# Kernel tuning notes

Hardware: AMD Instinct MI355X
Metric: run time of the kernel (lower is better)

Reference implementation:

```python
import jax, jax.numpy as jnp
import numpy as np

HEADS = 8
DIM_HEAD = 32
SCALE = DIM_HEAD ** -0.5


def setup_inputs() -> dict:
    key = jax.random.key(0)
    k1, k2, k3 = jax.random.split(key, 3)
    B, H, W, C = 16, 64, 64, 256
    hidden = HEADS * DIM_HEAD  # 256
    x = jax.random.normal(k1, (B, H, W, C), dtype=jnp.float32)
    # 1x1 convs with no bias == dense matmuls over channel dim (glorot-ish scale)
    w_qkv = jax.random.normal(k2, (C, 3 * hidden), dtype=jnp.float32) * (1.0 / np.sqrt(C))
    w_out = jax.random.normal(k3, (hidden, C), dtype=jnp.float32) * (1.0 / np.sqrt(hidden))
    return {"x": x, "w_qkv": w_qkv, "w_out": w_out}


def reference(x, w_qkv, w_out):
    B, H, W, C = x.shape
    n = H * W
    # to_qkv: 1x1 conv, no bias
    qkv = jnp.einsum('bhwc,cf->bhwf', x, w_qkv)  # [B,H,W,3*hidden]
    q, k, v = jnp.split(qkv, 3, axis=-1)

    def to_heads(t):
        # 'b x y (h c) -> b h c (x y)'
        t = t.reshape(B, n, HEADS, DIM_HEAD)
        return jnp.transpose(t, (0, 2, 3, 1))  # [B, heads, dim_head, n]

    q, k, v = to_heads(q), to_heads(k), to_heads(v)
    q = jax.nn.softmax(q, axis=-2) * SCALE      # softmax over feature dim d
    k = jax.nn.softmax(k, axis=-1)              # softmax over spatial dim n
    context = jnp.einsum('bhdn,bhen->bhde', k, v)   # [B, heads, d, e]
    out = jnp.einsum('bhde,bhdn->bhen', context, q)  # [B, heads, e, n]
    # 'b h c (x y) -> b x y (h c)'
    out = jnp.transpose(out, (0, 3, 1, 2)).reshape(B, H, W, HEADS * DIM_HEAD)
    # to_out: 1x1 conv, no bias
    return jnp.einsum('bhwf,fc->bhwc', out, w_out)
```

## Files before the change

kernel.cpp:

```cpp
#include <hip/hip_runtime.h>

using short8 = __attribute__((ext_vector_type(8))) short;
using f32x4  = __attribute__((ext_vector_type(4))) float;

#define SCALE_Q 0.17677669529663687f
#define NCHUNK 16

__device__ __forceinline__ unsigned short f2bf(float f) {
  unsigned u = __float_as_uint(f);
  return (unsigned short)((u + 0x7FFFu + ((u >> 16) & 1u)) >> 16);
}
__device__ __forceinline__ float bf2f(unsigned h) { return __uint_as_float(h << 16); }

__device__ __forceinline__ void bf8_to_f(uint4 r, float* o) {
  o[0] = bf2f(r.x & 0xffffu); o[1] = bf2f(r.x >> 16);
  o[2] = bf2f(r.y & 0xffffu); o[3] = bf2f(r.y >> 16);
  o[4] = bf2f(r.z & 0xffffu); o[5] = bf2f(r.z >> 16);
  o[6] = bf2f(r.w & 0xffffu); o[7] = bf2f(r.w >> 16);
}

__global__ __launch_bounds__(256) void prep_kernel(
    const float* __restrict__ x, const float* __restrict__ wqkv, const float* __restrict__ wout,
    unsigned short* __restrict__ xb, unsigned short* __restrict__ wqkvT,
    unsigned short* __restrict__ woutT) {
  const int blk = blockIdx.x;
  if (blk < 16384) {
    const size_t i = ((size_t)blk * 256 + threadIdx.x) * 4;
    const float4 v = *(const float4*)(x + i);
    *(ushort4*)(xb + i) = make_ushort4(f2bf(v.x), f2bf(v.y), f2bf(v.z), f2bf(v.w));
  } else if (blk < 16384 + 768) {
    const int n = blk - 16384, k = threadIdx.x;
    wqkvT[n * 256 + k] = f2bf(wqkv[(size_t)k * 768 + n]);
  } else {
    const int c = blk - 16384 - 768, f = threadIdx.x;
    woutT[c * 256 + f] = f2bf(wout[(size_t)f * 256 + c]);
  }
}

__global__ __launch_bounds__(256) void gemm_qkv(
    const unsigned short* __restrict__ A, const unsigned short* __restrict__ BT,
    unsigned short* __restrict__ KV, unsigned short* __restrict__ QS, int K) {
  __shared__ unsigned short As[2][128][40];
  __shared__ unsigned short Bs[2][128][40];
  const int cpx = (int)gridDim.x >> 3;
  const int lin = ((int)blockIdx.x & 7) * cpx + ((int)blockIdx.x >> 3);
  const int bn = lin % 6, bm = lin / 6;
  const int tid = threadIdx.x, lane = tid & 63, wid = tid >> 6;
  const int wr = wid >> 1, wc = wid & 1;
  const int fr = lane & 15, hi = lane >> 4, fk = hi * 8;
  f32x4 acc[4][4] = {};
  const size_t abase = (size_t)bm * 128 * K;
  const size_t bbase = (size_t)bn * 128 * K;

  const int srow = tid >> 2, skc = (tid & 3) * 8;
  uint4 ra0, ra1, rb0, rb1;
  const unsigned short* Ap = A + abase + (size_t)srow * K + skc;
  const unsigned short* Bp = BT + bbase + (size_t)srow * K + skc;

  ra0 = *(const uint4*)(Ap);            ra1 = *(const uint4*)(Ap + (size_t)64 * K);
  rb0 = *(const uint4*)(Bp);            rb1 = *(const uint4*)(Bp + (size_t)64 * K);
  *(uint4*)&As[0][srow][skc] = ra0;     *(uint4*)&As[0][srow + 64][skc] = ra1;
  *(uint4*)&Bs[0][srow][skc] = rb0;     *(uint4*)&Bs[0][srow + 64][skc] = rb1;
  __syncthreads();

  const int ktiles = K >> 5;
  int cur = 0;
  for (int t = 0; t < ktiles; ++t) {
    if (t + 1 < ktiles) {
      const int kt = (t + 1) * 32;
      ra0 = *(const uint4*)(Ap + kt);     ra1 = *(const uint4*)(Ap + (size_t)64 * K + kt);
      rb0 = *(const uint4*)(Bp + kt);     rb1 = *(const uint4*)(Bp + (size_t)64 * K + kt);
    }
    short8 af[4], bfv[4];
#pragma unroll
    for (int i = 0; i < 4; ++i) {
      af[i]  = *(const short8*)&As[cur][wr * 64 + i * 16 + fr][fk];
      bfv[i] = *(const short8*)&Bs[cur][wc * 64 + i * 16 + fr][fk];
    }
#pragma unroll
    for (int mi = 0; mi < 4; ++mi)
#pragma unroll
      for (int nj = 0; nj < 4; ++nj)
        acc[mi][nj] = __builtin_amdgcn_mfma_f32_16x16x32_bf16(bfv[nj], af[mi], acc[mi][nj], 0, 0, 0);
    if (t + 1 < ktiles) {
      *(uint4*)&As[cur ^ 1][srow][skc] = ra0;  *(uint4*)&As[cur ^ 1][srow + 64][skc] = ra1;
      *(uint4*)&Bs[cur ^ 1][srow][skc] = rb0;  *(uint4*)&Bs[cur ^ 1][srow + 64][skc] = rb1;
    }
    __syncthreads();
    cur ^= 1;
  }

  const size_t r0 = (size_t)bm * 128 + wr * 64;
  if (bn < 2) {
    const int c0 = bn * 128 + wc * 64;
#pragma unroll
    for (int mi = 0; mi < 4; ++mi) {
      const size_t row = r0 + mi * 16 + fr;
#pragma unroll
      for (int p = 0; p < 2; ++p) {
        const f32x4 a0 = acc[mi][2 * p], a1 = acc[mi][2 * p + 1];
        float mx = fmaxf(fmaxf(fmaxf(a0[0], a0[1]), fmaxf(a0[2], a0[3])),
                         fmaxf(fmaxf(a1[0], a1[1]), fmaxf(a1[2], a1[3])));
        mx = fmaxf(mx, __shfl_xor(mx, 16, 64));
        mx = fmaxf(mx, __shfl_xor(mx, 32, 64));
        float e0[4], e1[4], s = 0.f;
#pragma unroll
        for (int r = 0; r < 4; ++r) {
          e0[r] = __expf(a0[r] - mx); e1[r] = __expf(a1[r] - mx);
          s += e0[r] + e1[r];
        }
        s += __shfl_xor(s, 16, 64);
        s += __shfl_xor(s, 32, 64);
        const float inv = SCALE_Q / s;
        unsigned short* qp = QS + row * 256 + c0 + p * 32 + hi * 4;
        *(ushort4*)(qp)      = make_ushort4(f2bf(e0[0]*inv), f2bf(e0[1]*inv), f2bf(e0[2]*inv), f2bf(e0[3]*inv));
        *(ushort4*)(qp + 16) = make_ushort4(f2bf(e1[0]*inv), f2bf(e1[1]*inv), f2bf(e1[2]*inv), f2bf(e1[3]*inv));
      }
    }
    return;
  }
  const int colbase = (bn - 2) * 128 + wc * 64;
#pragma unroll
  for (int mi = 0; mi < 4; ++mi) {
    const size_t row = r0 + mi * 16 + fr;
#pragma unroll
    for (int nj = 0; nj < 4; ++nj) {
      const int col0 = colbase + nj * 16 + hi * 4;
      const f32x4 v = acc[mi][nj];
      *(ushort4*)(KV + row * 512 + col0) =
          make_ushort4(f2bf(v[0]), f2bf(v[1]), f2bf(v[2]), f2bf(v[3]));
    }
  }
}

__global__ __launch_bounds__(256) void gemm_out(
    const unsigned short* __restrict__ A, const unsigned short* __restrict__ BT,
    float* __restrict__ D, int K) {
  __shared__ unsigned short As[2][128][40];
  __shared__ unsigned short Bs[2][128][40];
  const int cpx = (int)gridDim.x >> 3;
  const int lin = ((int)blockIdx.x & 7) * cpx + ((int)blockIdx.x >> 3);
  const int bn = lin & 1, bm = (lin >> 1) & 31, bz = lin >> 6;
  const int tid = threadIdx.x, lane = tid & 63, wid = tid >> 6;
  const int wr = wid >> 1, wc = wid & 1;
  const int fr = lane & 15, hi = lane >> 4, fk = hi * 8;
  f32x4 acc[4][4] = {};
  const size_t abase = (size_t)bz * 4096 * 256 + (size_t)bm * 128 * K;
  const size_t bbase = (size_t)bz * 256 * 256 + (size_t)bn * 128 * K;

  const int srow = tid >> 2, skc = (tid & 3) * 8;
  uint4 ra0, ra1, rb0, rb1;
  const unsigned short* Ap = A + abase + (size_t)srow * K + skc;
  const unsigned short* Bp = BT + bbase + (size_t)srow * K + skc;

  ra0 = *(const uint4*)(Ap);            ra1 = *(const uint4*)(Ap + (size_t)64 * K);
  rb0 = *(const uint4*)(Bp);            rb1 = *(const uint4*)(Bp + (size_t)64 * K);
  *(uint4*)&As[0][srow][skc] = ra0;     *(uint4*)&As[0][srow + 64][skc] = ra1;
  *(uint4*)&Bs[0][srow][skc] = rb0;     *(uint4*)&Bs[0][srow + 64][skc] = rb1;
  __syncthreads();

  const int ktiles = K >> 5;
  int cur = 0;
  for (int t = 0; t < ktiles; ++t) {
    if (t + 1 < ktiles) {
      const int kt = (t + 1) * 32;
      ra0 = *(const uint4*)(Ap + kt);     ra1 = *(const uint4*)(Ap + (size_t)64 * K + kt);
      rb0 = *(const uint4*)(Bp + kt);     rb1 = *(const uint4*)(Bp + (size_t)64 * K + kt);
    }
    short8 af[4], bfv[4];
#pragma unroll
    for (int i = 0; i < 4; ++i) {
      af[i]  = *(const short8*)&As[cur][wr * 64 + i * 16 + fr][fk];
      bfv[i] = *(const short8*)&Bs[cur][wc * 64 + i * 16 + fr][fk];
    }
#pragma unroll
    for (int mi = 0; mi < 4; ++mi)
#pragma unroll
      for (int nj = 0; nj < 4; ++nj)
        acc[mi][nj] = __builtin_amdgcn_mfma_f32_16x16x32_bf16(bfv[nj], af[mi], acc[mi][nj], 0, 0, 0);
    if (t + 1 < ktiles) {
      *(uint4*)&As[cur ^ 1][srow][skc] = ra0;  *(uint4*)&As[cur ^ 1][srow + 64][skc] = ra1;
      *(uint4*)&Bs[cur ^ 1][srow][skc] = rb0;  *(uint4*)&Bs[cur ^ 1][srow + 64][skc] = rb1;
    }
    __syncthreads();
    cur ^= 1;
  }

  const size_t r0 = (size_t)bm * 128 + wr * 64;
  const int colbase = bn * 128 + wc * 64;
  float* Dz = D + (size_t)bz * 4096 * 256;
#pragma unroll
  for (int mi = 0; mi < 4; ++mi) {
    const size_t row = r0 + mi * 16 + fr;
#pragma unroll
    for (int nj = 0; nj < 4; ++nj) {
      const f32x4 v = acc[mi][nj];
      *(float4*)(Dz + row * 256 + colbase + nj * 16 + hi * 4) =
          make_float4(v[0], v[1], v[2], v[3]);
    }
  }
}

__global__ __launch_bounds__(256) void ctx_part_kernel(const unsigned short* __restrict__ kv,
                                                       float* __restrict__ part,
                                                       float* __restrict__ spart) {
  const int blk = blockIdx.x;
  const int bh = blk >> 4, chunk = blk & 15;
  const int b = bh >> 3, h = bh & 7;
  const int tid = threadIdx.x, d = tid & 31, g = tid >> 5;
  const unsigned short* kbase =
      kv + (size_t)b * 4096 * 512 + h * 32 + (size_t)chunk * 256 * 512;
  const unsigned short* vbase = kbase + 256;

  __shared__ float ek[64][36], vv[64][36];
  float a0 = 0.f, a1 = 0.f, a2 = 0.f, a3 = 0.f, ssum = 0.f;
  const int e0 = g * 4;
  const int sn = tid >> 2, sc = (tid & 3) * 8;
  const unsigned short* kp0 = kbase + (size_t)sn * 512 + sc;
  const unsigned short* vp0 = vbase + (size_t)sn * 512 + sc;
  uint4 kr = *(const uint4*)kp0;
  uint4 vr = *(const uint4*)vp0;
  for (int n0 = 0; n0 < 256; n0 += 64) {
    float kf[8], vf[8];
    bf8_to_f(kr, kf); bf8_to_f(vr, vf);
    uint4 krn = kr, vrn = vr;
    if (n0 + 64 < 256) {
      krn = *(const uint4*)(kp0 + (size_t)(n0 + 64) * 512);
      vrn = *(const uint4*)(vp0 + (size_t)(n0 + 64) * 512);
    }
#pragma unroll
    for (int j = 0; j < 8; ++j) { ek[sn][sc + j] = __expf(kf[j]); vv[sn][sc + j] = vf[j]; }
    __syncthreads();
#pragma unroll 8
    for (int i = 0; i < 64; ++i) {
      const float kd = ek[i][d];
      const float4 v4 = *(const float4*)&vv[i][e0];
      ssum += kd;
      a0 += kd * v4.x; a1 += kd * v4.y; a2 += kd * v4.z; a3 += kd * v4.w;
    }
    __syncthreads();
    kr = krn; vr = vrn;
  }
  float* pp = part + ((size_t)chunk * 128 + bh) * 1024 + d * 32 + e0;
  pp[0] = a0; pp[1] = a1; pp[2] = a2; pp[3] = a3;
  if (g == 0) spart[((size_t)chunk * 128 + bh) * 32 + d] = ssum;
}

__global__ __launch_bounds__(256) void ctx_combine_kernel(const float* __restrict__ part,
                                                          const float* __restrict__ spart,
                                                          float* __restrict__ ctx) {
  const int bh = blockIdx.x, tid = threadIdx.x;
  __shared__ float sinv[32];
  if (tid < 32) {
    float s = 0.f;
#pragma unroll
    for (int c = 0; c < NCHUNK; ++c) s += spart[((size_t)c * 128 + bh) * 32 + tid];
    sinv[tid] = 1.0f / s;
  }
  __syncthreads();
  float4 acc = make_float4(0.f, 0.f, 0.f, 0.f);
#pragma unroll
  for (int c = 0; c < NCHUNK; ++c) {
    const float4 p = *(const float4*)(part + ((size_t)c * 128 + bh) * 1024 + tid * 4);
    acc.x += p.x; acc.y += p.y; acc.z += p.z; acc.w += p.w;
  }
  const float si = sinv[tid >> 3];
  float4* cp = (float4*)(ctx + (size_t)bh * 1024 + tid * 4);
  *cp = make_float4(acc.x * si, acc.y * si, acc.z * si, acc.w * si);
}

__global__ __launch_bounds__(256) void w2_kernel(const float* __restrict__ ctx,
                                                 const unsigned short* __restrict__ woutT,
                                                 unsigned short* __restrict__ W2T) {
  const int b = blockIdx.x >> 4, cg = blockIdx.x & 15;
  const int tid = threadIdx.x;
  __shared__ float cs[8 * 32 * 32];
  {
    const float4* src = (const float4*)(ctx + (size_t)b * 8192);
    float4* dst = (float4*)cs;
#pragma unroll
    for (int i = 0; i < 8; ++i) dst[tid + i * 256] = src[tid + i * 256];
  }
  __syncthreads();
  const int c = cg * 16 + (tid >> 4), chunk = tid & 15;
  const int h = chunk >> 1, d0 = (chunk & 1) * 16;
  float wf[32];
  {
    const uint4* wp = (const uint4*)(woutT + (size_t)c * 256 + h * 32);
    bf8_to_f(wp[0], wf + 0); bf8_to_f(wp[1], wf + 8);
    bf8_to_f(wp[2], wf + 16); bf8_to_f(wp[3], wf + 24);
  }
  unsigned short o[16];
#pragma unroll
  for (int dd = 0; dd < 16; ++dd) {
    const float* cp = cs + h * 1024 + (d0 + dd) * 32;
    float acc = 0.f;
#pragma unroll
    for (int e = 0; e < 32; ++e) acc += cp[e] * wf[e];
    o[dd] = f2bf(acc);
  }
  uint4* op = (uint4*)(W2T + ((size_t)b * 256 + c) * 256 + chunk * 16);
  op[0] = make_uint4((unsigned)o[0] | ((unsigned)o[1] << 16), (unsigned)o[2] | ((unsigned)o[3] << 16),
                     (unsigned)o[4] | ((unsigned)o[5] << 16), (unsigned)o[6] | ((unsigned)o[7] << 16));
  op[1] = make_uint4((unsigned)o[8] | ((unsigned)o[9] << 16), (unsigned)o[10] | ((unsigned)o[11] << 16),
                     (unsigned)o[12] | ((unsigned)o[13] << 16), (unsigned)o[14] | ((unsigned)o[15] << 16));
}

extern "C" void kernel_launch(void* const* d_in, const int* in_sizes, int n_in,
                              void* d_out, int out_size, void* d_ws, size_t ws_size,
                              hipStream_t stream) {
  const float* x     = (const float*)d_in[0];
  const float* wqkv  = (const float*)d_in[1];
  const float* wout  = (const float*)d_in[2];
  float* out = (float*)d_out;

  char* ws = (char*)d_ws;
  unsigned short* xb    = (unsigned short*)(ws);
  unsigned short* wqkvT = (unsigned short*)(ws + 33554432);
  unsigned short* woutT = (unsigned short*)(ws + 33947648);
  unsigned short* kv    = (unsigned short*)(ws + 34078720);
  float*          ctx   = (float*)        (ws + 101187584);
  unsigned short* qs    = (unsigned short*)(ws + 101711872);
  float*          part  = (float*)(ws);
  float*          spart = (float*)(ws + 8388608);
  unsigned short* W2T   = (unsigned short*)(ws + 12582912);

  prep_kernel<<<16384 + 768 + 256, 256, 0, stream>>>(x, wqkv, wout, xb, wqkvT, woutT);
  gemm_qkv<<<3072, 256, 0, stream>>>(xb, wqkvT, kv, qs, 256);
  ctx_part_kernel<<<2048, 256, 0, stream>>>(kv, part, spart);
  ctx_combine_kernel<<<128, 256, 0, stream>>>(part, spart, ctx);
  w2_kernel<<<256, 256, 0, stream>>>(ctx, woutT, W2T);
  gemm_out<<<1024, 256, 0, stream>>>(qs, W2T, out, 256);
}
```

Measured before the change: 157.9 us.

## Load MFMA fragments directly from global memory, dropping LDS staging in GEMMs

Measured after the change: 218.4 us. 38.3% more time.

```diff
diff --git a/kernel.cpp b/kernel.cpp
--- a/kernel.cpp
+++ b/kernel.cpp
@@ -40,54 +40,40 @@
 __global__ __launch_bounds__(256) void gemm_qkv(
     const unsigned short* __restrict__ A, const unsigned short* __restrict__ BT,
     unsigned short* __restrict__ KV, unsigned short* __restrict__ QS, int K) {
-  __shared__ unsigned short As[2][128][40];
-  __shared__ unsigned short Bs[2][128][40];
   const int cpx = (int)gridDim.x >> 3;
   const int lin = ((int)blockIdx.x & 7) * cpx + ((int)blockIdx.x >> 3);
   const int bn = lin % 6, bm = lin / 6;
   const int tid = threadIdx.x, lane = tid & 63, wid = tid >> 6;
   const int wr = wid >> 1, wc = wid & 1;
-  const int fr = lane & 15, hi = lane >> 4, fk = hi * 8;
+  const int fr = lane & 15, hi = lane >> 4;
   f32x4 acc[4][4] = {};
-  const size_t abase = (size_t)bm * 128 * K;
-  const size_t bbase = (size_t)bn * 128 * K;
-
-  const int srow = tid >> 2, skc = (tid & 3) * 8;
-  uint4 ra0, ra1, rb0, rb1;
-  const unsigned short* Ap = A + abase + (size_t)srow * K + skc;
-  const unsigned short* Bp = BT + bbase + (size_t)srow * K + skc;
-
-  ra0 = *(const uint4*)(Ap);            ra1 = *(const uint4*)(Ap + (size_t)64 * K);
-  rb0 = *(const uint4*)(Bp);            rb1 = *(const uint4*)(Bp + (size_t)64 * K);
-  *(uint4*)&As[0][srow][skc] = ra0;     *(uint4*)&As[0][srow + 64][skc] = ra1;
-  *(uint4*)&Bs[0][srow][skc] = rb0;     *(uint4*)&Bs[0][srow + 64][skc] = rb1;
-  __syncthreads();
-
+
+  const unsigned short* ApA = A  + ((size_t)bm * 128 + wr * 64 + fr) * K + hi * 8;
+  const unsigned short* ApB = BT + ((size_t)bn * 128 + wc * 64 + fr) * K + hi * 8;
+
+  short8 ac[4], bc[4], an[4], bnx[4];
+#pragma unroll
+  for (int i = 0; i < 4; ++i) {
+    ac[i] = *(const short8*)(ApA + (size_t)i * 16 * K);
+    bc[i] = *(const short8*)(ApB + (size_t)i * 16 * K);
+  }
   const int ktiles = K >> 5;
-  int cur = 0;
   for (int t = 0; t < ktiles; ++t) {
     if (t + 1 < ktiles) {
       const int kt = (t + 1) * 32;
-      ra0 = *(const uint4*)(Ap + kt);     ra1 = *(const uint4*)(Ap + (size_t)64 * K + kt);
-      rb0 = *(const uint4*)(Bp + kt);     rb1 = *(const uint4*)(Bp + (size_t)64 * K + kt);
-    }
-    short8 af[4], bfv[4];
-#pragma unroll
-    for (int i = 0; i < 4; ++i) {
-      af[i]  = *(const short8*)&As[cur][wr * 64 + i * 16 + fr][fk];
-      bfv[i] = *(const short8*)&Bs[cur][wc * 64 + i * 16 + fr][fk];
+#pragma unroll
+      for (int i = 0; i < 4; ++i) {
+        an[i]  = *(const short8*)(ApA + (size_t)i * 16 * K + kt);
+        bnx[i] = *(const short8*)(ApB + (size_t)i * 16 * K + kt);
+      }
     }
 #pragma unroll
     for (int mi = 0; mi < 4; ++mi)
 #pragma unroll
       for (int nj = 0; nj < 4; ++nj)
-        acc[mi][nj] = __builtin_amdgcn_mfma_f32_16x16x32_bf16(bfv[nj], af[mi], acc[mi][nj], 0, 0, 0);
-    if (t + 1 < ktiles) {
-      *(uint4*)&As[cur ^ 1][srow][skc] = ra0;  *(uint4*)&As[cur ^ 1][srow + 64][skc] = ra1;
-      *(uint4*)&Bs[cur ^ 1][srow][skc] = rb0;  *(uint4*)&Bs[cur ^ 1][srow + 64][skc] = rb1;
-    }
-    __syncthreads();
-    cur ^= 1;
+        acc[mi][nj] = __builtin_amdgcn_mfma_f32_16x16x32_bf16(bc[nj], ac[mi], acc[mi][nj], 0, 0, 0);
+#pragma unroll
+    for (int i = 0; i < 4; ++i) { ac[i] = an[i]; bc[i] = bnx[i]; }
   }
 
   const size_t r0 = (size_t)bm * 128 + wr * 64;
@@ -136,54 +122,42 @@
 __global__ __launch_bounds__(256) void gemm_out(
     const unsigned short* __restrict__ A, const unsigned short* __restrict__ BT,
     float* __restrict__ D, int K) {
-  __shared__ unsigned short As[2][128][40];
-  __shared__ unsigned short Bs[2][128][40];
   const int cpx = (int)gridDim.x >> 3;
   const int lin = ((int)blockIdx.x & 7) * cpx + ((int)blockIdx.x >> 3);
   const int bn = lin & 1, bm = (lin >> 1) & 31, bz = lin >> 6;
   const int tid = threadIdx.x, lane = tid & 63, wid = tid >> 6;
   const int wr = wid >> 1, wc = wid & 1;
-  const int fr = lane & 15, hi = lane >> 4, fk = hi * 8;
+  const int fr = lane & 15, hi = lane >> 4;
   f32x4 acc[4][4] = {};
   const size_t abase = (size_t)bz * 4096 * 256 + (size_t)bm * 128 * K;
   const size_t bbase = (size_t)bz * 256 * 256 + (size_t)bn * 128 * K;
 
-  const int srow = tid >> 2, skc = (tid & 3) * 8;
-  uint4 ra0, ra1, rb0, rb1;
-  const unsigned short* Ap = A + abase + (size_t)srow * K + skc;
-  const unsigned short* Bp = BT + bbase + (size_t)srow * K + skc;
-
-  ra0 = *(const uint4*)(Ap);            ra1 = *(const uint4*)(Ap + (size_t)64 * K);
-  rb0 = *(const uint4*)(Bp);            rb1 = *(const uint4*)(Bp + (size_t)64 * K);
-  *(uint4*)&As[0][srow][skc] = ra0;     *(uint4*)&As[0][srow + 64][skc] = ra1;
-  *(uint4*)&Bs[0][srow][skc] = rb0;     *(uint4*)&Bs[0][srow + 64][skc] = rb1;
-  __syncthreads();
-
+  const unsigned short* ApA = A  + abase + ((size_t)wr * 64 + fr) * K + hi * 8;
+  const unsigned short* ApB = BT + bbase + ((size_t)wc * 64 + fr) * K + hi * 8;
+
+  short8 ac[4], bc[4], an[4], bnx[4];
+#pragma unroll
+  for (int i = 0; i < 4; ++i) {
+    ac[i] = *(const short8*)(ApA + (size_t)i * 16 * K);
+    bc[i] = *(const short8*)(ApB + (size_t)i * 16 * K);
+  }
   const int ktiles = K >> 5;
-  int cur = 0;
   for (int t = 0; t < ktiles; ++t) {
     if (t + 1 < ktiles) {
       const int kt = (t + 1) * 32;
-      ra0 = *(const uint4*)(Ap + kt);     ra1 = *(const uint4*)(Ap + (size_t)64 * K + kt);
-      rb0 = *(const uint4*)(Bp + kt);     rb1 = *(const uint4*)(Bp + (size_t)64 * K + kt);
-    }
-    short8 af[4], bfv[4];
-#pragma unroll
-    for (int i = 0; i < 4; ++i) {
-      af[i]  = *(const short8*)&As[cur][wr * 64 + i * 16 + fr][fk];
-      bfv[i] = *(const short8*)&Bs[cur][wc * 64 + i * 16 + fr][fk];
+#pragma unroll
+      for (int i = 0; i < 4; ++i) {
+        an[i]  = *(const short8*)(ApA + (size_t)i * 16 * K + kt);
+        bnx[i] = *(const short8*)(ApB + (size_t)i * 16 * K + kt);
+      }
     }
 #pragma unroll
     for (int mi = 0; mi < 4; ++mi)
 #pragma unroll
       for (int nj = 0; nj < 4; ++nj)
-        acc[mi][nj] = __builtin_amdgcn_mfma_f32_16x16x32_bf16(bfv[nj], af[mi], acc[mi][nj], 0, 0, 0);
-    if (t + 1 < ktiles) {
-      *(uint4*)&As[cur ^ 1][srow][skc] = ra0;  *(uint4*)&As[cur ^ 1][srow + 64][skc] = ra1;
-      *(uint4*)&Bs[cur ^ 1][srow][skc] = rb0;  *(uint4*)&Bs[cur ^ 1][srow + 64][skc] = rb1;
-    }
-    __syncthreads();
-    cur ^= 1;
+        acc[mi][nj] = __builtin_amdgcn_mfma_f32_16x16x32_bf16(bc[nj], ac[mi], acc[mi][nj], 0, 0, 0);
+#pragma unroll
+    for (int i = 0; i < 4; ++i) { ac[i] = an[i]; bc[i] = bnx[i]; }
   }
 
   const size_t r0 = (size_t)bm * 128 + wr * 64;
```
